# Kernel optimization log

Measured on AMD Instinct MI355X. Metric: run time of the kernel, lower is better.

## Reference

```python
import jax, jax.numpy as jnp
import numpy as np

N_NODES = 50000
IN_FEATS, H_FEATS, OUT_FEATS = 128, 128, 40
N_EDGES = 800000


def gcn_conv(x, src, dst, deg_inv_sqrt, W, b):
    # PyG GCNConv (eval): h = x @ W; msg = norm * h[src]; out = scatter_add(msg -> dst) + b
    h = x @ W  # [N, F_out]
    norm = deg_inv_sqrt[src] * deg_inv_sqrt[dst]  # [E+N] (self-loops included)
    msg = h[src] * norm[:, None]
    out = jax.ops.segment_sum(msg, dst, num_segments=x.shape[0])
    return out + b


def setup_inputs() -> dict:
    key = jax.random.key(0)
    k1, k2, k3, k4 = jax.random.split(key, 4)
    x = jax.random.normal(k1, (N_NODES, IN_FEATS), dtype=jnp.float32)
    edge_index = jax.random.randint(k2, (2, N_EDGES), 0, N_NODES, dtype=jnp.int64)
    # Glorot-ish init for weights, zeros for bias (PyG default)
    W1 = jax.random.normal(k3, (IN_FEATS, H_FEATS), dtype=jnp.float32) / np.sqrt(IN_FEATS)
    b1 = jnp.zeros((H_FEATS,), dtype=jnp.float32)
    W2 = jax.random.normal(k4, (H_FEATS, OUT_FEATS), dtype=jnp.float32) / np.sqrt(H_FEATS)
    b2 = jnp.zeros((OUT_FEATS,), dtype=jnp.float32)
    return {"x": x, "edge_index": edge_index, "W1": W1, "b1": b1, "W2": W2, "b2": b2}


def reference(x, edge_index, W1, b1, W2, b2):
    n = x.shape[0]
    loop = jnp.arange(n, dtype=edge_index.dtype)
    src = jnp.concatenate([edge_index[0], loop])  # add self-loops
    dst = jnp.concatenate([edge_index[1], loop])
    # symmetric normalization: deg over destinations (incl. self-loops)
    deg = jnp.zeros((n,), dtype=x.dtype).at[dst].add(1.0)
    deg_inv_sqrt = jnp.where(deg > 0, jax.lax.rsqrt(deg), 0.0)
    # dropout(p=0.6) is identity in eval mode
    h = jax.nn.relu(gcn_conv(x, src, dst, deg_inv_sqrt, W1, b1))
    out = gcn_conv(h, src, dst, deg_inv_sqrt, W2, b2)
    return out
```

## Files before the change

### kernel.cpp

```cpp
#include <hip/hip_runtime.h>
#include <hip/hip_fp16.h>

#define THREADS 256
#define EPB 2048
#define LDK 136

using f16x8 = __attribute__((ext_vector_type(8))) _Float16;
using f32x4 = __attribute__((ext_vector_type(4))) float;

__global__ __launch_bounds__(256) void k_wcvt(const float* __restrict__ W1,
                                              const float* __restrict__ W2,
                                              __half* __restrict__ wt1,
                                              __half* __restrict__ wt2) {
    const int idx = blockIdx.x * 256 + threadIdx.x;
    if (idx < 128 * 128) {
        const int nn = idx >> 7, kk = idx & 127;
        wt1[idx] = __float2half(W1[kk * 128 + nn]);
    } else {
        const int o = idx - 128 * 128;
        if (o < 48 * 128) {
            const int nn = o >> 7, kk = o & 127;
            wt2[o] = (nn < 40) ? __float2half(W2[kk * 40 + nn]) : __half(0.f);
        }
    }
}


__global__ __launch_bounds__(256) void k_hist(const int* __restrict__ dst,
                                              int* __restrict__ Hmat,
                                              int e, int nbuck, int nbpad) {
    __shared__ int h[256];
    const int t = threadIdx.x;
    h[t] = 0;
    __syncthreads();
    const int base4 = blockIdx.x * 512;
#pragma unroll
    for (int k = 0; k < 2; ++k) {
        const int i4 = base4 + k * 256 + t;
        const int i = i4 * 4;
        if (i + 3 < e) {
            const int4 d4 = ((const int4*)dst)[i4];
            atomicAdd(&h[d4.x >> 8], 1);
            atomicAdd(&h[d4.y >> 8], 1);
            atomicAdd(&h[d4.z >> 8], 1);
            atomicAdd(&h[d4.w >> 8], 1);
        } else {
            for (int j = i; j < e; ++j) atomicAdd(&h[dst[j] >> 8], 1);
        }
    }
    __syncthreads();
    if (t < nbuck) Hmat[t * nbpad + blockIdx.x] = h[t];
}

__global__ __launch_bounds__(256) void k_bscan(const int* __restrict__ Hmat,
                                               int* __restrict__ Off,
                                               int* __restrict__ btot,
                                               int nb, int nbpad) {
    __shared__ int s[256];
    const int b = blockIdx.x, t = threadIdx.x;
    const int* H = Hmat + b * nbpad;
    const int v0 = (2 * t     < nb) ? H[2 * t]     : 0;
    const int v1 = (2 * t + 1 < nb) ? H[2 * t + 1] : 0;
    const int p = v0 + v1;
    s[t] = p;
    __syncthreads();
    for (int off = 1; off < 256; off <<= 1) {
        int w = (t >= off) ? s[t - off] : 0;
        __syncthreads();
        s[t] += w;
        __syncthreads();
    }
    const int excl = s[t] - p;
    int* O = Off + b * nbpad;
    if (2 * t     < nb) O[2 * t]     = excl;
    if (2 * t + 1 < nb) O[2 * t + 1] = excl + v0;
    if (t == 255) btot[b] = s[255];
}

__global__ __launch_bounds__(256) void k_scat(const int* __restrict__ src,
                                              const int* __restrict__ dst,
                                              const int* __restrict__ Off,
                                              const int* __restrict__ btot,
                                              int2* __restrict__ sorted,
                                              int e, int nbuck, int nbpad) {
    __shared__ int h[256];
    __shared__ int sc[256];
    __shared__ int comb[256];
    const int t = threadIdx.x;
    const int v = (t < nbuck) ? btot[t] : 0;
    h[t] = 0;
    sc[t] = v;
    __syncthreads();
    for (int off = 1; off < 256; off <<= 1) {
        int w = (t >= off) ? sc[t - off] : 0;
        __syncthreads();
        sc[t] += w;
        __syncthreads();
    }
    comb[t] = (sc[t] - v) + ((t < nbuck) ? Off[t * nbpad + blockIdx.x] : 0);
    __syncthreads();

    const int base4 = blockIdx.x * 512;
#pragma unroll
    for (int k = 0; k < 2; ++k) {
        const int i4 = base4 + k * 256 + t;
        const int i = i4 * 4;
        if (i + 3 < e) {
            const int4 s4 = ((const int4*)src)[i4];
            const int4 d4 = ((const int4*)dst)[i4];
            {
                const int b = d4.x >> 8;
                sorted[comb[b] + atomicAdd(&h[b], 1)] = make_int2(s4.x, d4.x);
            }
            {
                const int b = d4.y >> 8;
                sorted[comb[b] + atomicAdd(&h[b], 1)] = make_int2(s4.y, d4.y);
            }
            {
                const int b = d4.z >> 8;
                sorted[comb[b] + atomicAdd(&h[b], 1)] = make_int2(s4.z, d4.z);
            }
            {
                const int b = d4.w >> 8;
                sorted[comb[b] + atomicAdd(&h[b], 1)] = make_int2(s4.w, d4.w);
            }
        } else {
            for (int j = i; j < e; ++j) {
                const int d = dst[j];
                const int b = d >> 8;
                sorted[comb[b] + atomicAdd(&h[b], 1)] = make_int2(src[j], d);
            }
        }
    }
}

__global__ __launch_bounds__(256) void k_bsort(const int2* __restrict__ sorted,
                                               const int* __restrict__ btot,
                                               int* __restrict__ csr_src,
                                               int* __restrict__ rowptr,
                                               float* __restrict__ dinv,
                                               int n, int nbuck, int e) {
    __shared__ int cnt[256];
    __shared__ int s[256];
    __shared__ int fil[256];
    const int b = blockIdx.x, t = threadIdx.x;

    const int v = (t < nbuck) ? btot[t] : 0;
    s[t] = v;
    cnt[t] = 0;
    __syncthreads();
    for (int off = 1; off < 256; off <<= 1) {
        int w = (t >= off) ? s[t - off] : 0;
        __syncthreads();
        s[t] += w;
        __syncthreads();
    }
    const int hi = s[b];
    const int lo = hi - btot[b];
    __syncthreads();

    for (int p = lo + t; p < hi; p += 256) atomicAdd(&cnt[sorted[p].y & 255], 1);
    __syncthreads();
    const int c = cnt[t];
    s[t] = c;
    __syncthreads();
    for (int off = 1; off < 256; off <<= 1) {
        int w = (t >= off) ? s[t - off] : 0;
        __syncthreads();
        s[t] += w;
        __syncthreads();
    }
    const int excl = s[t] - c;
    const int node = b * 256 + t;
    if (node < n) {
        rowptr[node] = lo + excl;
        dinv[node] = rsqrtf((float)(c + 1));
    }
    if (b == 0 && t == 0) rowptr[n] = e;
    fil[t] = lo + excl;
    __syncthreads();
    for (int p = lo + t; p < hi; p += 256) {
        const int2 pr = sorted[p];
        const int pos = atomicAdd(&fil[pr.y & 255], 1);
        csr_src[pos] = pr.x;
    }
}

__global__ __launch_bounds__(256) void k_gemm1(const float* __restrict__ x,
                                               const __half* __restrict__ wt1,
                                               const float* __restrict__ dinv,
                                               __half* __restrict__ g, int n) {
    __shared__ _Float16 Wt[128 * LDK];
    __shared__ _Float16 xl[64 * LDK];
    const int t  = threadIdx.x;
    const int wv = t >> 6;
    const int l  = t & 63;
    const int base = blockIdx.x * 64;

    {
        const uint4* Wg = (const uint4*)wt1;
#pragma unroll
        for (int i = 0; i < 8; ++i) {
            const int idx = t + 256 * i;
            const int row = idx >> 4, c8 = idx & 15;
            *(uint4*)(Wt + row * LDK + c8 * 8) = Wg[idx];
        }
    }
#pragma unroll
    for (int i = 0; i < 8; ++i) {
        const int idx = t + 256 * i;
        const int r = idx >> 5, c4 = idx & 31;
        const int row = base + r;
        float4 v = make_float4(0.f, 0.f, 0.f, 0.f);
        if (row < n) v = *(const float4*)(x + (size_t)row * 128 + c4 * 4);
        union { __half2 h2[2]; uint2 u; } pk;
        pk.h2[0] = __floats2half2_rn(v.x, v.y);
        pk.h2[1] = __floats2half2_rn(v.z, v.w);
        *(uint2*)(xl + r * LDK + c4 * 4) = pk.u;
    }
    __syncthreads();

    f32x4 acc[8];
#pragma unroll
    for (int i = 0; i < 8; ++i) acc[i] = (f32x4){0.f, 0.f, 0.f, 0.f};

    const int arow = wv * 16 + (l & 15);
    const int koff = (l >> 4) * 8;
#pragma unroll
    for (int kb = 0; kb < 4; ++kb) {
        const f16x8 a = *(const f16x8*)(xl + arow * LDK + kb * 32 + koff);
#pragma unroll
        for (int nt = 0; nt < 8; ++nt) {
            const f16x8 b = *(const f16x8*)(Wt + (nt * 16 + (l & 15)) * LDK + kb * 32 + koff);
            acc[nt] = __builtin_amdgcn_mfma_f32_16x16x32_f16(a, b, acc[nt], 0, 0, 0);
        }
    }

#pragma unroll
    for (int i = 0; i < 4; ++i) {
        const int row = base + wv * 16 + (l >> 4) * 4 + i;
        if (row < n) {
            const float dv = dinv[row];
#pragma unroll
            for (int nt = 0; nt < 8; ++nt)
                g[(size_t)row * 128 + nt * 16 + (l & 15)] = __float2half(acc[nt][i] * dv);
        }
    }
}

__global__ __launch_bounds__(256) void k_gather1(const __half2* __restrict__ g,
                                                 const int* __restrict__ rowptr,
                                                 const int* __restrict__ csr_src,
                                                 const float* __restrict__ dinv,
                                                 const float* __restrict__ b1,
                                                 __half2* __restrict__ out1, int n) {
    const int wave = threadIdx.x >> 6;
    const int lane = threadIdx.x & 63;
    const int d = blockIdx.x * 4 + wave;
    if (d >= n) return;
    const int beg = rowptr[d], end = rowptr[d + 1];
    float ax = 0.f, ay = 0.f, bx = 0.f, by = 0.f;
    int p = beg;
    for (; p + 4 <= end; p += 4) {
        const int s0 = csr_src[p],     s1 = csr_src[p + 1];
        const int s2 = csr_src[p + 2], s3 = csr_src[p + 3];
        const __half2 v0 = g[(size_t)s0 * 64 + lane];
        const __half2 v1 = g[(size_t)s1 * 64 + lane];
        const __half2 v2 = g[(size_t)s2 * 64 + lane];
        const __half2 v3 = g[(size_t)s3 * 64 + lane];
        const float2 f0 = __half22float2(v0), f1 = __half22float2(v1);
        const float2 f2 = __half22float2(v2), f3 = __half22float2(v3);
        ax += f0.x + f2.x; ay += f0.y + f2.y;
        bx += f1.x + f3.x; by += f1.y + f3.y;
    }
    for (; p < end; ++p) {
        const int s0 = csr_src[p];
        const float2 f0 = __half22float2(g[(size_t)s0 * 64 + lane]);
        ax += f0.x; ay += f0.y;
    }
    const float2 fs = __half22float2(g[(size_t)d * 64 + lane]);
    ax += bx + fs.x;
    ay += by + fs.y;
    const float dd = dinv[d];
    const float2 bb = *(const float2*)(b1 + lane * 2);
    const float rx = fmaxf(fmaf(dd, ax, bb.x), 0.f);
    const float ry = fmaxf(fmaf(dd, ay, bb.y), 0.f);
    out1[(size_t)d * 64 + lane] = __floats2half2_rn(rx, ry);
}

__global__ __launch_bounds__(256) void k_gemm2(const __half* __restrict__ h1,
                                               const __half* __restrict__ wt2,
                                               const float* __restrict__ dinv,
                                               __half* __restrict__ g, int n) {
    __shared__ _Float16 Wt[48 * LDK];
    __shared__ _Float16 xl[64 * LDK];
    const int t  = threadIdx.x;
    const int wv = t >> 6;
    const int l  = t & 63;
    const int base = blockIdx.x * 64;

    {
        const uint4* Wg = (const uint4*)wt2;
#pragma unroll
        for (int i = 0; i < 3; ++i) {
            const int idx = t + 256 * i;
            const int row = idx >> 4, c8 = idx & 15;
            *(uint4*)(Wt + row * LDK + c8 * 8) = Wg[idx];
        }
    }
#pragma unroll
    for (int i = 0; i < 4; ++i) {
        const int idx = t + 256 * i;
        const int r = idx >> 4, c8 = idx & 15;
        const int row = base + r;
        uint4 v = make_uint4(0u, 0u, 0u, 0u);
        if (row < n) v = *(const uint4*)(h1 + (size_t)row * 128 + c8 * 8);
        *(uint4*)(xl + r * LDK + c8 * 8) = v;
    }
    __syncthreads();

    f32x4 acc[3];
#pragma unroll
    for (int i = 0; i < 3; ++i) acc[i] = (f32x4){0.f, 0.f, 0.f, 0.f};

    const int arow = wv * 16 + (l & 15);
    const int koff = (l >> 4) * 8;
#pragma unroll
    for (int kb = 0; kb < 4; ++kb) {
        const f16x8 a = *(const f16x8*)(xl + arow * LDK + kb * 32 + koff);
#pragma unroll
        for (int nt = 0; nt < 3; ++nt) {
            const f16x8 b = *(const f16x8*)(Wt + (nt * 16 + (l & 15)) * LDK + kb * 32 + koff);
            acc[nt] = __builtin_amdgcn_mfma_f32_16x16x32_f16(a, b, acc[nt], 0, 0, 0);
        }
    }

#pragma unroll
    for (int i = 0; i < 4; ++i) {
        const int row = base + wv * 16 + (l >> 4) * 4 + i;
        if (row < n) {
            const float dv = dinv[row];
#pragma unroll
            for (int nt = 0; nt < 3; ++nt) {
                const int col = nt * 16 + (l & 15);
                if (col < 40)
                    g[(size_t)row * 40 + col] = __float2half(acc[nt][i] * dv);
            }
        }
    }
}

__global__ __launch_bounds__(256) void k_gather2(const __half2* __restrict__ g,
                                                 const int* __restrict__ rowptr,
                                                 const int* __restrict__ csr_src,
                                                 const float* __restrict__ dinv,
                                                 const float* __restrict__ b2,
                                                 float* __restrict__ out, int n) {
    const int wave = threadIdx.x >> 6;
    const int lane = threadIdx.x & 63;
    const int d = blockIdx.x * 4 + wave;
    if (d >= n) return;
    const int eg = lane / 20;
    const int f  = lane - eg * 20;
    const int beg = rowptr[d], end = rowptr[d + 1];
    float ax = 0.f, ay = 0.f;
    if (eg < 3) {
        for (int p = beg + eg; p < end; p += 3) {
            const int s0 = csr_src[p];
            const float2 f0 = __half22float2(g[(size_t)s0 * 20 + f]);
            ax += f0.x; ay += f0.y;
        }
    }
    ax += __shfl(ax, lane + 20) + __shfl(ax, lane + 40);
    ay += __shfl(ay, lane + 20) + __shfl(ay, lane + 40);
    if (lane < 20) {
        const float2 fs = __half22float2(g[(size_t)d * 20 + lane]);
        ax += fs.x; ay += fs.y;
        const float dd = dinv[d];
        const float2 bb = *(const float2*)(b2 + lane * 2);
        float2 r;
        r.x = fmaf(dd, ax, bb.x);
        r.y = fmaf(dd, ay, bb.y);
        *(float2*)(out + (size_t)d * 40 + lane * 2) = r;
    }
}

extern "C" void kernel_launch(void* const* d_in, const int* in_sizes, int n_in,
                              void* d_out, int out_size, void* d_ws, size_t ws_size,
                              hipStream_t stream) {
    const float* x  = (const float*)d_in[0];
    const int*   ei = (const int*)d_in[1];
    const float* W1 = (const float*)d_in[2];
    const float* b1 = (const float*)d_in[3];
    const float* W2 = (const float*)d_in[4];
    const float* b2 = (const float*)d_in[5];
    float* out = (float*)d_out;

    const int n = in_sizes[0] / 128;
    const int e = in_sizes[1] / 2;
    const int* src = ei;
    const int* dst = ei + e;

    const int n_pad = ((n + 63) / 64) * 64;
    const int e_pad = ((e + 63) / 64) * 64;
    const int NB    = (e + EPB - 1) / EPB;
    const int nbuck = (n + 255) >> 8;
    const int nbpad = ((NB + 63) / 64) * 64;

    float*   ws      = (float*)d_ws;
    float*   dinv    = ws;
    int*     rowptr  = (int*)(ws + n_pad);
    int*     csr_src = rowptr + n_pad + 64;
    __half2* g1      = (__half2*)(csr_src + e_pad);
    __half*  out1h   = (__half*)(g1 + (size_t)n_pad * 64);
    __half*  wt1h    = out1h + (size_t)n_pad * 128;
    __half*  wt2h    = wt1h + 128 * 128;
    int2*    sorted  = (int2*)g1;
    int*     Hmat    = (int*)g1 + (size_t)e_pad * 2;
    int*     Off     = Hmat + nbuck * nbpad;
    int*     btot    = Off + nbuck * nbpad;
    __half2* g2      = g1;

    const int nb_rows = (n + 63) / 64;
    const int nb_g    = (n + 3) / 4;

    k_wcvt<<<(128 * 128 + 48 * 128 + 255) / 256, 256, 0, stream>>>(W1, W2, wt1h, wt2h);

    k_hist <<<NB,    256, 0, stream>>>(dst, Hmat, e, nbuck, nbpad);
    k_bscan<<<nbuck, 256, 0, stream>>>(Hmat, Off, btot, NB, nbpad);
    k_scat <<<NB,    256, 0, stream>>>(src, dst, Off, btot, sorted, e, nbuck, nbpad);
    k_bsort<<<nbuck, 256, 0, stream>>>(sorted, btot, csr_src, rowptr, dinv, n, nbuck, e);

    k_gemm1  <<<nb_rows, 256, 0, stream>>>(x, wt1h, dinv, (__half*)g1, n);
    k_gather1<<<nb_g, 256, 0, stream>>>(g1, rowptr, csr_src, dinv, b1, (__half2*)out1h, n);

    k_gemm2  <<<nb_rows, 256, 0, stream>>>(out1h, wt2h, dinv, (__half*)g2, n);
    k_gather2<<<nb_g, 256, 0, stream>>>(g2, rowptr, csr_src, dinv, b2, out, n);
}
```

Baseline: 130.4 us.

## Pack sorted edges into one int and slab the layer-1 gather by feature

```diff
diff --git a/kernel.cpp b/kernel.cpp
--- a/kernel.cpp
+++ b/kernel.cpp
@@ -81,7 +81,7 @@
                                               const int* __restrict__ dst,
                                               const int* __restrict__ Off,
                                               const int* __restrict__ btot,
-                                              int2* __restrict__ sorted,
+                                              int* __restrict__ sorted,
                                               int e, int nbuck, int nbpad) {
     __shared__ int h[256];
     __shared__ int sc[256];
@@ -110,31 +110,31 @@
             const int4 d4 = ((const int4*)dst)[i4];
             {
                 const int b = d4.x >> 8;
-                sorted[comb[b] + atomicAdd(&h[b], 1)] = make_int2(s4.x, d4.x);
+                sorted[comb[b] + atomicAdd(&h[b], 1)] = (s4.x << 8) | (d4.x & 255);
             }
             {
                 const int b = d4.y >> 8;
-                sorted[comb[b] + atomicAdd(&h[b], 1)] = make_int2(s4.y, d4.y);
+                sorted[comb[b] + atomicAdd(&h[b], 1)] = (s4.y << 8) | (d4.y & 255);
             }
             {
                 const int b = d4.z >> 8;
-                sorted[comb[b] + atomicAdd(&h[b], 1)] = make_int2(s4.z, d4.z);
+                sorted[comb[b] + atomicAdd(&h[b], 1)] = (s4.z << 8) | (d4.z & 255);
             }
             {
                 const int b = d4.w >> 8;
-                sorted[comb[b] + atomicAdd(&h[b], 1)] = make_int2(s4.w, d4.w);
+                sorted[comb[b] + atomicAdd(&h[b], 1)] = (s4.w << 8) | (d4.w & 255);
             }
         } else {
             for (int j = i; j < e; ++j) {
                 const int d = dst[j];
                 const int b = d >> 8;
-                sorted[comb[b] + atomicAdd(&h[b], 1)] = make_int2(src[j], d);
-            }
-        }
-    }
-}
-
-__global__ __launch_bounds__(256) void k_bsort(const int2* __restrict__ sorted,
+                sorted[comb[b] + atomicAdd(&h[b], 1)] = (src[j] << 8) | (d & 255);
+            }
+        }
+    }
+}
+
+__global__ __launch_bounds__(256) void k_bsort(const int* __restrict__ sorted,
                                                const int* __restrict__ btot,
                                                int* __restrict__ csr_src,
                                                int* __restrict__ rowptr,
@@ -159,7 +159,7 @@
     const int lo = hi - btot[b];
     __syncthreads();
 
-    for (int p = lo + t; p < hi; p += 256) atomicAdd(&cnt[sorted[p].y & 255], 1);
+    for (int p = lo + t; p < hi; p += 256) atomicAdd(&cnt[sorted[p] & 255], 1);
     __syncthreads();
     const int c = cnt[t];
     s[t] = c;
@@ -180,22 +180,23 @@
     fil[t] = lo + excl;
     __syncthreads();
     for (int p = lo + t; p < hi; p += 256) {
-        const int2 pr = sorted[p];
-        const int pos = atomicAdd(&fil[pr.y & 255], 1);
-        csr_src[pos] = pr.x;
+        const int pr = sorted[p];
+        const int pos = atomicAdd(&fil[pr & 255], 1);
+        csr_src[pos] = pr >> 8;
     }
 }
 
 __global__ __launch_bounds__(256) void k_gemm1(const float* __restrict__ x,
                                                const __half* __restrict__ wt1,
                                                const float* __restrict__ dinv,
-                                               __half* __restrict__ g, int n) {
+                                               __half* __restrict__ g, int n, int n_pad) {
     __shared__ _Float16 Wt[128 * LDK];
     __shared__ _Float16 xl[64 * LDK];
     const int t  = threadIdx.x;
     const int wv = t >> 6;
     const int l  = t & 63;
     const int base = blockIdx.x * 64;
+    const size_t slabstride = (size_t)n_pad * 32;
 
     {
         const uint4* Wg = (const uint4*)wt1;
@@ -243,7 +244,8 @@
             const float dv = dinv[row];
 #pragma unroll
             for (int nt = 0; nt < 8; ++nt)
-                g[(size_t)row * 128 + nt * 16 + (l & 15)] = __float2half(acc[nt][i] * dv);
+                g[(nt >> 1) * slabstride + (size_t)row * 32 + (nt & 1) * 16 + (l & 15)] =
+                    __float2half(acc[nt][i] * dv);
         }
     }
 }
@@ -253,39 +255,43 @@
                                                  const int* __restrict__ csr_src,
                                                  const float* __restrict__ dinv,
                                                  const float* __restrict__ b1,
-                                                 __half2* __restrict__ out1, int n) {
+                                                 __half2* __restrict__ out1,
+                                                 int n, int n_pad) {
     const int wave = threadIdx.x >> 6;
     const int lane = threadIdx.x & 63;
     const int d = blockIdx.x * 4 + wave;
     if (d >= n) return;
+    const int y  = blockIdx.y;
+    const int f  = lane & 15;
+    const int eg = lane >> 4;
+    const __half2* gs = g + (size_t)y * n_pad * 16;
     const int beg = rowptr[d], end = rowptr[d + 1];
     float ax = 0.f, ay = 0.f, bx = 0.f, by = 0.f;
-    int p = beg;
-    for (; p + 4 <= end; p += 4) {
-        const int s0 = csr_src[p],     s1 = csr_src[p + 1];
-        const int s2 = csr_src[p + 2], s3 = csr_src[p + 3];
-        const __half2 v0 = g[(size_t)s0 * 64 + lane];
-        const __half2 v1 = g[(size_t)s1 * 64 + lane];
-        const __half2 v2 = g[(size_t)s2 * 64 + lane];
-        const __half2 v3 = g[(size_t)s3 * 64 + lane];
-        const float2 f0 = __half22float2(v0), f1 = __half22float2(v1);
-        const float2 f2 = __half22float2(v2), f3 = __half22float2(v3);
-        ax += f0.x + f2.x; ay += f0.y + f2.y;
-        bx += f1.x + f3.x; by += f1.y + f3.y;
-    }
-    for (; p < end; ++p) {
+    int p = beg + eg;
+    for (; p + 4 < end; p += 8) {
+        const int s0 = csr_src[p], s1 = csr_src[p + 4];
+        const float2 f0 = __half22float2(gs[(size_t)s0 * 16 + f]);
+        const float2 f1 = __half22float2(gs[(size_t)s1 * 16 + f]);
+        ax += f0.x; ay += f0.y;
+        bx += f1.x; by += f1.y;
+    }
+    for (; p < end; p += 4) {
         const int s0 = csr_src[p];
-        const float2 f0 = __half22float2(g[(size_t)s0 * 64 + lane]);
+        const float2 f0 = __half22float2(gs[(size_t)s0 * 16 + f]);
         ax += f0.x; ay += f0.y;
     }
-    const float2 fs = __half22float2(g[(size_t)d * 64 + lane]);
-    ax += bx + fs.x;
-    ay += by + fs.y;
-    const float dd = dinv[d];
-    const float2 bb = *(const float2*)(b1 + lane * 2);
-    const float rx = fmaxf(fmaf(dd, ax, bb.x), 0.f);
-    const float ry = fmaxf(fmaf(dd, ay, bb.y), 0.f);
-    out1[(size_t)d * 64 + lane] = __floats2half2_rn(rx, ry);
+    ax += bx; ay += by;
+    ax += __shfl_xor(ax, 16); ay += __shfl_xor(ay, 16);
+    ax += __shfl_xor(ax, 32); ay += __shfl_xor(ay, 32);
+    if (eg == 0) {
+        const float2 fs = __half22float2(gs[(size_t)d * 16 + f]);
+        ax += fs.x; ay += fs.y;
+        const float dd = dinv[d];
+        const float2 bb = *(const float2*)(b1 + y * 32 + f * 2);
+        const float rx = fmaxf(fmaf(dd, ax, bb.x), 0.f);
+        const float ry = fmaxf(fmaf(dd, ay, bb.y), 0.f);
+        out1[(size_t)d * 64 + y * 16 + f] = __floats2half2_rn(rx, ry);
+    }
 }
 
 __global__ __launch_bounds__(256) void k_gemm2(const __half* __restrict__ h1,
@@ -411,15 +417,15 @@
     float*   dinv    = ws;
     int*     rowptr  = (int*)(ws + n_pad);
     int*     csr_src = rowptr + n_pad + 64;
-    __half2* g1      = (__half2*)(csr_src + e_pad);
-    __half*  out1h   = (__half*)(g1 + (size_t)n_pad * 64);
+    __half*  g1      = (__half*)(csr_src + e_pad);
+    __half*  out1h   = g1 + (size_t)n_pad * 128;
     __half*  wt1h    = out1h + (size_t)n_pad * 128;
     __half*  wt2h    = wt1h + 128 * 128;
-    int2*    sorted  = (int2*)g1;
-    int*     Hmat    = (int*)g1 + (size_t)e_pad * 2;
+    int*     sorted  = (int*)g1;
+    int*     Hmat    = (int*)g1 + e_pad;
     int*     Off     = Hmat + nbuck * nbpad;
     int*     btot    = Off + nbuck * nbpad;
-    __half2* g2      = g1;
+    __half2* g2      = (__half2*)g1;
 
     const int nb_rows = (n + 63) / 64;
     const int nb_g    = (n + 3) / 4;
@@ -431,8 +437,9 @@
     k_scat <<<NB,    256, 0, stream>>>(src, dst, Off, btot, sorted, e, nbuck, nbpad);
     k_bsort<<<nbuck, 256, 0, stream>>>(sorted, btot, csr_src, rowptr, dinv, n, nbuck, e);
 
-    k_gemm1  <<<nb_rows, 256, 0, stream>>>(x, wt1h, dinv, (__half*)g1, n);
-    k_gather1<<<nb_g, 256, 0, stream>>>(g1, rowptr, csr_src, dinv, b1, (__half2*)out1h, n);
+    k_gemm1  <<<nb_rows, 256, 0, stream>>>(x, wt1h, dinv, g1, n, n_pad);
+    k_gather1<<<dim3(nb_g, 4), 256, 0, stream>>>((const __half2*)g1, rowptr, csr_src,
+                                                 dinv, b1, (__half2*)out1h, n, n_pad);
 
     k_gemm2  <<<nb_rows, 256, 0, stream>>>(out1h, wt2h, dinv, (__half*)g2, n);
     k_gather2<<<nb_g, 256, 0, stream>>>(g2, rowptr, csr_src, dinv, b2, out, n);
```

Measured after the change: 169.4 us. 29.9% more time.
